# Kernel tuning notes

Measured on AMD Instinct MI355X. Metric: run time of the kernel, lower is better.

## Reference

```python
import jax, jax.numpy as jnp
import numpy as np

BS, NQ, NH, HD = 4, 10000, 8, 32   # batch, queries, heads, head_dim
NP = 4                              # sampling points
H, W = 100, 100                     # fixed spatial shape (value_spatial_shapes_list[0])


def grid_sample_bilinear_zeros(img, grid):
    """PyTorch F.grid_sample(mode='bilinear', padding_mode='zeros', align_corners=False).
    img: (N, C, Hin, Win); grid: (N, Hg, Wg, 2) with (x, y) in [-1, 1].
    Returns (N, C, Hg, Wg)."""
    N, C, Hin, Win = img.shape
    Hg, Wg = grid.shape[1], grid.shape[2]
    # unnormalize (align_corners=False)
    x = (grid[..., 0] + 1.0) * (Win * 0.5) - 0.5
    y = (grid[..., 1] + 1.0) * (Hin * 0.5) - 0.5
    x0 = jnp.floor(x); y0 = jnp.floor(y)
    x1 = x0 + 1.0;     y1 = y0 + 1.0
    wx1 = x - x0; wx0 = 1.0 - wx1
    wy1 = y - y0; wy0 = 1.0 - wy1
    img_flat = img.reshape(N, C, Hin * Win)

    def gather(xi, yi, w):
        xi_i = xi.astype(jnp.int32); yi_i = yi.astype(jnp.int32)
        valid = (xi_i >= 0) & (xi_i < Win) & (yi_i >= 0) & (yi_i < Hin)
        xc = jnp.clip(xi_i, 0, Win - 1); yc = jnp.clip(yi_i, 0, Hin - 1)
        idx = (yc * Win + xc).reshape(N, 1, Hg * Wg)
        vals = jnp.take_along_axis(img_flat, idx, axis=2)      # (N, C, Hg*Wg)
        wm = jnp.where(valid, w, 0.0).reshape(N, 1, Hg * Wg)
        return vals * wm

    out = (gather(x0, y0, wx0 * wy0) + gather(x1, y0, wx1 * wy0)
           + gather(x0, y1, wx0 * wy1) + gather(x1, y1, wx1 * wy1))
    return out.reshape(N, C, Hg, Wg)


def setup_inputs() -> dict:
    key = jax.random.key(0)
    k1, k2, k3 = jax.random.split(key, 3)
    value = jax.random.normal(k1, (BS, H * W, NH, HD), dtype=jnp.float32)
    value_spatial_shapes = jnp.array([[H, W]], dtype=jnp.int64)  # unused (fixed-size variant)
    sampling_locations = jax.random.uniform(k2, (BS, NQ, NH, 1, NP, 2), dtype=jnp.float32)
    attention_weights = jax.random.uniform(k3, (BS, NQ, NH, 1, NP), dtype=jnp.float32)
    return {"value": value, "value_spatial_shapes": value_spatial_shapes,
            "sampling_locations": sampling_locations, "attention_weights": attention_weights}


def reference(value, value_spatial_shapes, sampling_locations, attention_weights):
    bs, _, nh, d = value.shape
    nq, npnt = sampling_locations.shape[1], sampling_locations.shape[4]
    # (bs, HW, nh, d) -> (bs*nh, d, H, W)
    v = jnp.transpose(value, (0, 2, 3, 1)).reshape(bs * nh, d, H, W)
    # sampling grids in [-1, 1]; single level -> index 0
    grids = 2.0 * sampling_locations[:, :, :, 0] - 1.0           # (bs, nq, nh, np, 2)
    grids = jnp.transpose(grids, (0, 2, 1, 3, 4)).reshape(bs * nh, nq, npnt, 2)
    sampled = grid_sample_bilinear_zeros(v, grids)               # (bs*nh, d, nq, np)
    aw = jnp.transpose(attention_weights, (0, 2, 1, 3, 4)).reshape(bs * nh, 1, nq, npnt)
    out = (sampled * aw).sum(-1)                                 # (bs*nh, d, nq)
    out = out.reshape(bs, nh * d, nq)
    return jnp.transpose(out, (0, 2, 1))                         # (bs, nq, nh*d)
```

## Files before the change

### kernel.cpp

```cpp
#include <hip/hip_runtime.h>


constexpr int BS = 4, NQ = 10000, NH = 8, HD = 32, NP = 4, H = 100, W = 100;
constexpr int HW = H * W;
constexpr unsigned VBYTES_F32 = (unsigned)BS * HW * NH * HD * 4u;
constexpr unsigned VH_BYTES   = (unsigned)BS * HW * NH * HD * 2u;

typedef float    f32x4 __attribute__((ext_vector_type(4)));
typedef float    f32x8 __attribute__((ext_vector_type(8)));
typedef _Float16 f16x8 __attribute__((ext_vector_type(8)));
typedef unsigned u32x4 __attribute__((ext_vector_type(4)));

__global__ __launch_bounds__(256)
void cast_kernel(const float* __restrict__ v, _Float16* __restrict__ vh)
{
    const int tid = blockIdx.x * 256 + (int)threadIdx.x;
    const int c8 = tid & 3;
    const int t2 = tid >> 2;
    const int x  = t2 % 100;
    const int t3 = t2 / 100;
    const int y  = t3 % 100;
    const int t4 = t3 / 100;
    const float* src = v + ((size_t)(t4 >> 3) * HW + y * W + x) * 256 + (t4 & 7) * 32 + c8 * 8;
    const f32x4 a = __builtin_nontemporal_load((const f32x4*)src);
    const f32x4 b = __builtin_nontemporal_load((const f32x4*)(src + 4));
    const f32x8 f = {a.x, a.y, a.z, a.w, b.x, b.y, b.z, b.w};
    const f16x8 o = __builtin_convertvector(f, f16x8);
    *(f16x8*)(vh + ((size_t)t4 * HW + y * W + x) * 32 + c8 * 8) = o;
}

__global__ __launch_bounds__(256, 4)
void gather_kernel(const _Float16* __restrict__ vh,
                   const float* __restrict__ sloc,
                   const float* __restrict__ aw,
                   float* __restrict__ out)
{
    const int chunk = gridDim.x >> 3;
    const int swz   = (blockIdx.x & 7) * chunk + (blockIdx.x >> 3);

    const int tid   = swz * 256 + (int)threadIdx.x;
    const int group = tid >> 3;
    const int lane  = tid & 7;
    const int xsel  = lane >> 2;
    const int csel  = lane & 3;

    const int q  = group % NQ;
    const int bh = group / NQ;
    const int h  = bh & (NH - 1);
    const int b  = bh >> 3;
    const int bq = b * NQ + q;

    const size_t pbase = (size_t)bq * NH + h;
    const f32x4 l01 = *(const f32x4*)(sloc + pbase * (NP * 2));
    const f32x4 l23 = *(const f32x4*)(sloc + pbase * (NP * 2) + 4);
    const f32x4 wv  = *(const f32x4*)(aw   + pbase * NP);

    const float lx[NP] = {l01.x, l01.z, l23.x, l23.z};
    const float ly[NP] = {l01.y, l01.w, l23.y, l23.w};
    const float wp[NP] = {wv.x,  wv.y,  wv.z,  wv.w};

    const unsigned slabbase = (unsigned)(bh * HW) * 64u;

    unsigned voff[NP][2];
    float    wrow[NP][2];
    float    wxl[NP];
#pragma unroll
    for (int p = 0; p < NP; ++p) {
        const float x = lx[p] * (float)W - 0.5f;
        const float y = ly[p] * (float)H - 0.5f;
        const float x0f = floorf(x);
        const float y0f = floorf(y);
        const int   x0  = (int)x0f, y0 = (int)y0f;
        const float fx1 = x - x0f, fx0 = 1.f - fx1;
        const float fy1 = y - y0f, fy0 = 1.f - fy1;

        const int xc = x0 + xsel;
        wxl[p] = ((unsigned)xc < (unsigned)W) ? (xsel ? fx1 : fx0) * wp[p] : 0.f;
        wrow[p][0] = ((unsigned)y0 < (unsigned)H)       ? fy0 : 0.f;
        wrow[p][1] = ((unsigned)(y0 + 1) < (unsigned)H) ? fy1 : 0.f;

        const int basex = min(max(x0, 0), W - 2);
        const int sl    = min(max(xc, 0), W - 1) - basex;
        const int y0c   = min(max(y0, 0), H - 1);
        const int y1c   = min(max(y0 + 1, 0), H - 1);
        const unsigned lo = (unsigned)(basex) * 64u + (unsigned)sl * 64u + (unsigned)csel * 16u;
        voff[p][0] = slabbase + (unsigned)(y0c * W) * 64u + lo;
        voff[p][1] = slabbase + (unsigned)(y1c * W) * 64u + lo;
    }

    union { const _Float16* p; unsigned u[2]; } va; va.p = vh;
    const u32x4 rsrc = {va.u[0], va.u[1] & 0xFFFFu, VH_BYTES, 0x00020000u};

    f32x4 r00, r01, r10, r11, r20, r21, r30, r31;
#define GLOAD(dst, off) \
    asm volatile("buffer_load_dwordx4 %0, %1, %2, 0 offen" \
                 : "=v"(dst) : "v"(off), "s"(rsrc))
    GLOAD(r00, voff[0][0]); GLOAD(r01, voff[0][1]);
    GLOAD(r10, voff[1][0]); GLOAD(r11, voff[1][1]);
    GLOAD(r20, voff[2][0]); GLOAD(r21, voff[2][1]);
    GLOAD(r30, voff[3][0]); GLOAD(r31, voff[3][1]);
#undef GLOAD

    f32x8 acc = (f32x8)(0.f);
#define CONSUME(ra, rb, p, cnt) \
    asm volatile("s_waitcnt vmcnt(" #cnt ")" : "+v"(ra), "+v"(rb)); \
    { const f32x8 v0 = __builtin_convertvector(__builtin_bit_cast(f16x8, ra), f32x8); \
      const f32x8 v1 = __builtin_convertvector(__builtin_bit_cast(f16x8, rb), f32x8); \
      acc += v0 * (wxl[p] * wrow[p][0]) + v1 * (wxl[p] * wrow[p][1]); }
    CONSUME(r00, r01, 0, 6)
    CONSUME(r10, r11, 1, 4)
    CONSUME(r20, r21, 2, 2)
    CONSUME(r30, r31, 3, 0)
#undef CONSUME

    f32x8 other;
#pragma unroll
    for (int j = 0; j < 8; ++j) other[j] = __shfl_xor(acc[j], 4, 8);
    acc += other;

    const f32x4 res = xsel ? (f32x4){acc[4], acc[5], acc[6], acc[7]}
                           : (f32x4){acc[0], acc[1], acc[2], acc[3]};
    __builtin_nontemporal_store(res,
        (f32x4*)(out + (size_t)bq * (NH * HD) + h * HD + csel * 8 + xsel * 4));
}

__global__ __launch_bounds__(256, 4)
void deform_attn_f32(const float* __restrict__ value,
                     const float* __restrict__ sloc,
                     const float* __restrict__ aw,
                     float* __restrict__ out)
{
    const int chunk = gridDim.x >> 3;
    const int swz   = (blockIdx.x & 7) * chunk + (blockIdx.x >> 3);
    const int tid   = swz * 256 + (int)threadIdx.x;
    const int group = tid >> 3;
    const int lane  = tid & 7;
    const int q  = group % NQ;
    const int bh = group / NQ;
    const int h  = bh & (NH - 1);
    const int b  = bh >> 3;
    const int bq = b * NQ + q;
    const size_t pbase = (size_t)bq * NH + h;
    const f32x4 l01 = *(const f32x4*)(sloc + pbase * (NP * 2));
    const f32x4 l23 = *(const f32x4*)(sloc + pbase * (NP * 2) + 4);
    const f32x4 wv  = *(const f32x4*)(aw   + pbase * NP);
    const float lx[NP] = {l01.x, l01.z, l23.x, l23.z};
    const float ly[NP] = {l01.y, l01.w, l23.y, l23.w};
    const float wp[NP] = {wv.x,  wv.y,  wv.z,  wv.w};
    const float* vbase = value + (size_t)b * HW * NH * HD + h * HD + lane * 4;
    f32x4 acc = (f32x4)(0.f);
#pragma unroll
    for (int p = 0; p < NP; ++p) {
        const float x = lx[p] * (float)W - 0.5f;
        const float y = ly[p] * (float)H - 0.5f;
        const float x0f = floorf(x), y0f = floorf(y);
        const int x0 = (int)x0f, y0 = (int)y0f, x1 = x0 + 1, y1 = y0 + 1;
        const float wx1 = x - x0f, wx0 = 1.f - wx1, wy1 = y - y0f, wy0 = 1.f - wy1;
        const bool vx0 = (unsigned)x0 < (unsigned)W, vx1 = (unsigned)x1 < (unsigned)W;
        const bool vy0 = (unsigned)y0 < (unsigned)H, vy1 = (unsigned)y1 < (unsigned)H;
        const int xc0 = min(max(x0, 0), W - 1), xc1 = min(max(x1, 0), W - 1);
        const int yc0 = min(max(y0, 0), H - 1), yc1 = min(max(y1, 0), H - 1);
        const float w00 = (vx0 && vy0) ? wp[p] * wx0 * wy0 : 0.f;
        const float w10 = (vx1 && vy0) ? wp[p] * wx1 * wy0 : 0.f;
        const float w01 = (vx0 && vy1) ? wp[p] * wx0 * wy1 : 0.f;
        const float w11 = (vx1 && vy1) ? wp[p] * wx1 * wy1 : 0.f;
        const f32x4 v00 = *(const f32x4*)(vbase + (size_t)(yc0 * W + xc0) * (NH * HD));
        const f32x4 v10 = *(const f32x4*)(vbase + (size_t)(yc0 * W + xc1) * (NH * HD));
        const f32x4 v01 = *(const f32x4*)(vbase + (size_t)(yc1 * W + xc0) * (NH * HD));
        const f32x4 v11 = *(const f32x4*)(vbase + (size_t)(yc1 * W + xc1) * (NH * HD));
        acc += w00 * v00 + w10 * v10 + w01 * v01 + w11 * v11;
    }
    __builtin_nontemporal_store(acc, (f32x4*)(out + (size_t)bq * (NH * HD) + h * HD + lane * 4));
}

extern "C" void kernel_launch(void* const* d_in, const int* in_sizes, int n_in,
                              void* d_out, int out_size, void* d_ws, size_t ws_size,
                              hipStream_t stream) {
    const float* value = (const float*)d_in[0];
    const float* sloc  = (const float*)d_in[2];
    const float* aw    = (const float*)d_in[3];
    float*       out   = (float*)d_out;

    if (ws_size >= (size_t)VH_BYTES) {
        _Float16* vh = (_Float16*)d_ws;
        cast_kernel<<<5000, 256, 0, stream>>>(value, vh);
        gather_kernel<<<10000, 256, 0, stream>>>(vh, sloc, aw, out);
    } else {
        deform_attn_f32<<<10000, 256, 0, stream>>>(value, sloc, aw, out);
    }
}
```

Measured before the change: 125.0 us.

## Store each fp16 pixel paired with its right neighbour to co-locate bilinear x-taps

The cast kernel now writes a duplicated fp16 layout in which each pixel's 128-byte record holds its own 32 channels followed by those of its right neighbour (clamped at the edge). The gather kernel addresses this layout so that both horizontal taps of a bilinear sample sit in one contiguous 128-byte record, rather than spanning two adjacent pixels that may cross cache-line boundaries. This is meant to reduce the cache lines touched per sample row. In exchange the workspace doubles in size and the cast kernel writes twice as many bytes.

```diff
diff --git a/kernel.cpp b/kernel.cpp
--- a/kernel.cpp
+++ b/kernel.cpp
@@ -3,8 +3,7 @@
 
 constexpr int BS = 4, NQ = 10000, NH = 8, HD = 32, NP = 4, H = 100, W = 100;
 constexpr int HW = H * W;
-constexpr unsigned VBYTES_F32 = (unsigned)BS * HW * NH * HD * 4u;
-constexpr unsigned VH_BYTES   = (unsigned)BS * HW * NH * HD * 2u;
+constexpr unsigned VH_BYTES = (unsigned)BS * NH * HW * 128u;
 
 typedef float    f32x4 __attribute__((ext_vector_type(4)));
 typedef float    f32x8 __attribute__((ext_vector_type(8)));
@@ -12,21 +11,31 @@
 typedef unsigned u32x4 __attribute__((ext_vector_type(4)));
 
 __global__ __launch_bounds__(256)
-void cast_kernel(const float* __restrict__ v, _Float16* __restrict__ vh)
+void cast_dup_kernel(const float* __restrict__ v, _Float16* __restrict__ vh)
 {
-    const int tid = blockIdx.x * 256 + (int)threadIdx.x;
-    const int c8 = tid & 3;
-    const int t2 = tid >> 2;
-    const int x  = t2 % 100;
-    const int t3 = t2 / 100;
-    const int y  = t3 % 100;
-    const int t4 = t3 / 100;
-    const float* src = v + ((size_t)(t4 >> 3) * HW + y * W + x) * 256 + (t4 & 7) * 32 + c8 * 8;
-    const f32x4 a = __builtin_nontemporal_load((const f32x4*)src);
-    const f32x4 b = __builtin_nontemporal_load((const f32x4*)(src + 4));
-    const f32x8 f = {a.x, a.y, a.z, a.w, b.x, b.y, b.z, b.w};
-    const f16x8 o = __builtin_convertvector(f, f16x8);
-    *(f16x8*)(vh + ((size_t)t4 * HW + y * W + x) * 32 + c8 * 8) = o;
+    const int tid  = blockIdx.x * 256 + (int)threadIdx.x;
+    const int half = tid & 1;
+    const int t2   = tid >> 1;
+    const int x    = t2 % W;
+    const int t3   = t2 / W;
+    const int y    = t3 % H;
+    const int bh   = t3 / H;
+    const int px   = min(x + half, W - 1);
+
+    const float* src = v + ((size_t)(bh >> 3) * HW + (size_t)(y * W + px)) * (NH * HD)
+                         + (bh & 7) * HD;
+    f16x8 o[4];
+#pragma unroll
+    for (int i = 0; i < 4; ++i) {
+        const f32x4 a = *(const f32x4*)(src + i * 8);
+        const f32x4 c = *(const f32x4*)(src + i * 8 + 4);
+        const f32x8 f = {a.x, a.y, a.z, a.w, c.x, c.y, c.z, c.w};
+        o[i] = __builtin_convertvector(f, f16x8);
+    }
+    _Float16* dst = vh + (size_t)t2 * 64 + half * 32;
+#pragma unroll
+    for (int i = 0; i < 4; ++i)
+        *(f16x8*)(dst + i * 8) = o[i];
 }
 
 __global__ __launch_bounds__(256, 4)
@@ -59,7 +68,7 @@
     const float ly[NP] = {l01.y, l01.w, l23.y, l23.w};
     const float wp[NP] = {wv.x,  wv.y,  wv.z,  wv.w};
 
-    const unsigned slabbase = (unsigned)(bh * HW) * 64u;
+    const unsigned slabbase = (unsigned)(bh * HW) * 128u;
 
     unsigned voff[NP][2];
     float    wrow[NP][2];
@@ -79,13 +88,13 @@
         wrow[p][0] = ((unsigned)y0 < (unsigned)H)       ? fy0 : 0.f;
         wrow[p][1] = ((unsigned)(y0 + 1) < (unsigned)H) ? fy1 : 0.f;
 
-        const int basex = min(max(x0, 0), W - 2);
+        const int basex = min(max(x0, 0), W - 1);
         const int sl    = min(max(xc, 0), W - 1) - basex;
         const int y0c   = min(max(y0, 0), H - 1);
         const int y1c   = min(max(y0 + 1, 0), H - 1);
-        const unsigned lo = (unsigned)(basex) * 64u + (unsigned)sl * 64u + (unsigned)csel * 16u;
-        voff[p][0] = slabbase + (unsigned)(y0c * W) * 64u + lo;
-        voff[p][1] = slabbase + (unsigned)(y1c * W) * 64u + lo;
+        const unsigned lo = (unsigned)sl * 64u + (unsigned)csel * 16u;
+        voff[p][0] = slabbase + (unsigned)(y0c * W + basex) * 128u + lo;
+        voff[p][1] = slabbase + (unsigned)(y1c * W + basex) * 128u + lo;
     }
 
     union { const _Float16* p; unsigned u[2]; } va; va.p = vh;
@@ -183,7 +192,7 @@
 
     if (ws_size >= (size_t)VH_BYTES) {
         _Float16* vh = (_Float16*)d_ws;
-        cast_kernel<<<5000, 256, 0, stream>>>(value, vh);
+        cast_dup_kernel<<<2500, 256, 0, stream>>>(value, vh);
         gather_kernel<<<10000, 256, 0, stream>>>(vh, sloc, aw, out);
     } else {
         deform_attn_f32<<<10000, 256, 0, stream>>>(value, sloc, aw, out);
```

Measured after the change: 135.2 us. 8.2% more time.
